# Performance work log

Measured on AMD Instinct MI355X. Metric: run time of the kernel, lower is better.

Reference implementation:

```python
import jax, jax.numpy as jnp
import numpy as np

B, C, T = 128, 272, 1024
D1, K = 270, 32


def setup_inputs() -> dict:
    key = jax.random.key(0)
    k1, k2, k3, k4 = jax.random.split(key, 4)
    X = jax.random.normal(k1, (B, C, T), dtype=jnp.float32)
    loc = jax.random.uniform(k2, (C, 2), dtype=jnp.float32)  # 2D sensor coords in [0,1]
    z_re = jax.random.normal(k3, (D1, K, K), dtype=jnp.float32)
    z_im = jax.random.normal(k4, (D1, K, K), dtype=jnp.float32)
    return {"X": X, "loc": loc, "z_re": z_re, "z_im": z_im}


def reference(X, loc, z_re, z_im):
    # X: [B, C, T]; loc: [C, 2]; z_re/z_im: [D1, K, K]
    Kdim = z_re.shape[1]
    x, y = loc[:, 0], loc[:, 1]                      # [C]
    k = jnp.arange(Kdim, dtype=X.dtype)
    # phase[k, l, c] = 2*pi*(k*x[c] + l*y[c])
    phase = 2.0 * jnp.pi * (k[:, None, None] * x[None, None, :]
                            + k[None, :, None] * y[None, None, :])  # [K, K, C]
    # a[j, c] = sum_{k,l} z_re[j,k,l]*cos(phase) + z_im[j,k,l]*sin(phase)
    A = (jnp.einsum('dkl,klc->dc', z_re, jnp.cos(phase))
         + jnp.einsum('dkl,klc->dc', z_im, jnp.sin(phase)))  # [D1, C]
    # exp(a_j) / sum_c exp(a_j) == softmax over channels (same math)
    w = jax.nn.softmax(A, axis=1)                    # [D1, C]
    # out[b, j, t] = sum_c w[j,c] * X[b,c,t]
    return jnp.einsum('dc,bct->bdt', w, X)           # [B, D1, T]
```

## Files before the change

### kernel.cpp

```cpp
#include <hip/hip_runtime.h>

#define BB 128
#define CC 272
#define TT 1024
#define DD 270
#define KK 32
#define NKC 9
#define MP 272
#define NT 256
#define WCH (CC * KK)
#define WBYTES (NKC * WCH * 2)

typedef __attribute__((ext_vector_type(8))) short s16x8;
typedef __attribute__((ext_vector_type(4))) float f32x4;

__device__ __forceinline__ unsigned short f2bf(float f) {
  unsigned int u = __builtin_bit_cast(unsigned int, f);
  u += 0x7fffu + ((u >> 16) & 1u);
  return (unsigned short)(u >> 16);
}

__global__ __launch_bounds__(288) void phaseA_kernel(
    const float* __restrict__ loc, const float* __restrict__ z_re,
    const float* __restrict__ z_im, float* __restrict__ A) {
  const int d = blockIdx.x;
  const int p = blockIdx.y;
  const int c = threadIdx.x;
  if (c >= CC) return;
  const float TWO_PI = 6.28318530717958647692f;
  float x = loc[2 * c], y = loc[2 * c + 1];
  float sx, cx, sy, cyv;
  sincosf(TWO_PI * x, &sx, &cx);
  sincosf(TWO_PI * y, &sy, &cyv);
  float cl[KK], sl[KK];
  cl[0] = 1.f; sl[0] = 0.f;
#pragma unroll
  for (int l = 1; l < KK; ++l) {
    cl[l] = cl[l - 1] * cyv - sl[l - 1] * sy;
    sl[l] = sl[l - 1] * cyv + cl[l - 1] * sy;
  }
  const int k0 = p * 8;
  float sk, ck;
  sincosf(TWO_PI * (float)k0 * x, &sk, &ck);
  const float* zr = z_re + (size_t)d * (KK * KK) + k0 * KK;
  const float* zi = z_im + (size_t)d * (KK * KK) + k0 * KK;
  float acc = 0.f;
  for (int k = 0; k < 8; ++k) {
    float s_rc = 0.f, s_rs = 0.f, s_ic = 0.f, s_is = 0.f;
#pragma unroll
    for (int l = 0; l < KK; ++l) {
      float vr = zr[k * KK + l];
      float vi = zi[k * KK + l];
      s_rc += vr * cl[l];
      s_rs += vr * sl[l];
      s_ic += vi * cl[l];
      s_is += vi * sl[l];
    }
    acc += ck * (s_rc + s_is) + sk * (s_ic - s_rs);
    float nck = ck * cx - sk * sx;
    sk = sk * cx + ck * sx;
    ck = nck;
  }
  atomicAdd(&A[d * CC + c], acc);
}

__global__ __launch_bounds__(64) void softmax_kernel(
    const float* __restrict__ A, unsigned short* __restrict__ wb) {
  const int d = blockIdx.x;
  const int lane = threadIdx.x;
  const bool live = (d < DD);
  float v[5];
  float inv = 0.f;
  if (live) {
    float m = -3.0e38f;
#pragma unroll
    for (int j = 0; j < 5; ++j) {
      int cidx = lane + 64 * j;
      v[j] = (cidx < CC) ? A[(size_t)d * CC + cidx] : -3.0e38f;
      m = fmaxf(m, v[j]);
    }
#pragma unroll
    for (int off = 32; off >= 1; off >>= 1) m = fmaxf(m, __shfl_xor(m, off, 64));
    float s = 0.f;
#pragma unroll
    for (int j = 0; j < 5; ++j) {
      int cidx = lane + 64 * j;
      v[j] = (cidx < CC) ? expf(v[j] - m) : 0.f;
      s += v[j];
    }
#pragma unroll
    for (int off = 32; off >= 1; off >>= 1) s += __shfl_xor(s, off, 64);
    inv = 1.f / s;
  }
#pragma unroll
  for (int j = 0; j < 5; ++j) {
    int kk = lane + 64 * j;
    if (kk < NKC * KK) {
      unsigned short val = 0;
      if (live && kk < CC) val = f2bf(v[j] * inv);
      int kc = kk >> 5, ks = kk & 31, s = ks >> 3, o = ks & 7;
      wb[(size_t)kc * WCH + d * KK + ((s ^ (d & 3)) << 3) + o] = val;
    }
  }
}

__global__ __launch_bounds__(1024) void gemm_kernel(
    const float* __restrict__ X, const unsigned short* __restrict__ wb,
    float* __restrict__ out) {
  __shared__ unsigned short wlds[NKC * WCH];
  const int bid = blockIdx.x;
  const int b = bid >> 2;
  const int t0 = (bid & 3) * NT;
  const int tid = threadIdx.x;
  const int lane = tid & 63;
  const int wv = tid >> 6;
  const int q = lane >> 4;
  const int r16 = lane & 15;

  {
    const char* src = (const char*)wb;
    char* dst = (char*)wlds;
#pragma unroll
    for (int r = 0; r < 10; ++r) {
      int idx = tid + r * 1024;
      if (idx < WBYTES / 16) {
        __builtin_amdgcn_global_load_lds(
            (const __attribute__((address_space(1))) unsigned int*)(src + idx * 16),
            (__attribute__((address_space(3))) unsigned int*)(dst + idx * 16),
            16, 0, 0);
      }
    }
  }

  f32x4 acc[17];
#pragma unroll
  for (int i = 0; i < 17; ++i) acc[i] = (f32x4){0.f, 0.f, 0.f, 0.f};

  const float* Xb = X + (size_t)b * (CC * TT) + t0 + wv * 16 + r16;
  const int csub = q * 8;
  const int base_l = r16 * 64 + ((q ^ (r16 & 3)) << 4);

  float xf[8];
#pragma unroll
  for (int j = 0; j < 8; ++j) xf[j] = Xb[(size_t)(csub + j) * TT];

  __syncthreads();

  for (int kc = 0; kc < NKC; ++kc) {
    float xn[8];
    if (kc < NKC - 1) {
      const int cbase = (kc + 1) * KK + csub;
#pragma unroll
      for (int j = 0; j < 8; ++j)
        xn[j] = (cbase + j < CC) ? Xb[(size_t)(cbase + j) * TT] : 0.f;
    } else {
#pragma unroll
      for (int j = 0; j < 8; ++j) xn[j] = 0.f;
    }
    union { unsigned int u[4]; s16x8 v; } bf;
#pragma unroll
    for (int j2 = 0; j2 < 4; ++j2)
      bf.u[j2] = (unsigned int)f2bf(xf[2 * j2]) |
                 ((unsigned int)f2bf(xf[2 * j2 + 1]) << 16);
    const char* wchunk = (const char*)wlds + kc * (WCH * 2);
#pragma unroll
    for (int mt = 0; mt < 17; ++mt) {
      s16x8 afrag = *(const s16x8*)(wchunk + mt * 1024 + base_l);
      acc[mt] = __builtin_amdgcn_mfma_f32_16x16x32_bf16(afrag, bf.v, acc[mt], 0, 0, 0);
    }
#pragma unroll
    for (int j = 0; j < 8; ++j) xf[j] = xn[j];
  }

  float* op = out + (size_t)b * (DD * TT) + t0 + wv * 16 + r16;
#pragma unroll
  for (int mt = 0; mt < 17; ++mt) {
#pragma unroll
    for (int r = 0; r < 4; ++r) {
      int drow = mt * 16 + q * 4 + r;
      if (drow < DD) op[(size_t)drow * TT] = acc[mt][r];
    }
  }
}

extern "C" void kernel_launch(void* const* d_in, const int* in_sizes, int n_in,
                              void* d_out, int out_size, void* d_ws, size_t ws_size,
                              hipStream_t stream) {
  const float* X = (const float*)d_in[0];
  const float* loc = (const float*)d_in[1];
  const float* z_re = (const float*)d_in[2];
  const float* z_im = (const float*)d_in[3];
  float* out = (float*)d_out;

  float* A = (float*)d_ws;
  unsigned short* wbf = (unsigned short*)((char*)d_ws + 294912);

  hipMemsetAsync(A, 0, DD * CC * sizeof(float), stream);
  phaseA_kernel<<<dim3(DD, 4), 288, 0, stream>>>(loc, z_re, z_im, A);
  softmax_kernel<<<MP, 64, 0, stream>>>(A, wbf);
  gemm_kernel<<<BB * (TT / NT), 1024, 0, stream>>>(X, wbf, out);
}
```

Baseline: 314.5 us.

## Process two T-tiles per GEMM block and store weights in MFMA fragment order

Each GEMM block now covers 512 time steps as two sequential 256-wide passes, so the bf16 weight matrix is staged into LDS half as often (256 blocks instead of 512). The softmax kernel writes the weights already laid out in MFMA A-fragment order, which turns each LDS read into a contiguous lane*16 access with no XOR swizzle. Between the two passes the accumulators are flushed to global memory. The grid now has 256 blocks, so it barely covers the CU count and leaves less room for overlap across blocks.

Result: slower. 369.4 us (+17.5%).

```diff
diff --git a/kernel.cpp b/kernel.cpp
--- a/kernel.cpp
+++ b/kernel.cpp
@@ -7,8 +7,7 @@
 #define KK 32
 #define NKC 9
 #define MP 272
-#define NT 256
-#define WCH (CC * KK)
+#define WCH (MP * KK)
 #define WBYTES (NKC * WCH * 2)
 
 typedef __attribute__((ext_vector_type(8))) short s16x8;
@@ -92,14 +91,15 @@
     for (int off = 32; off >= 1; off >>= 1) s += __shfl_xor(s, off, 64);
     inv = 1.f / s;
   }
+  const int mt = d >> 4, r = d & 15;
 #pragma unroll
   for (int j = 0; j < 5; ++j) {
     int kk = lane + 64 * j;
     if (kk < NKC * KK) {
       unsigned short val = 0;
       if (live && kk < CC) val = f2bf(v[j] * inv);
-      int kc = kk >> 5, ks = kk & 31, s = ks >> 3, o = ks & 7;
-      wb[(size_t)kc * WCH + d * KK + ((s ^ (d & 3)) << 3) + o] = val;
+      int kc = kk >> 5, q = (kk >> 3) & 3, jj = kk & 7;
+      wb[(size_t)kc * WCH + mt * 512 + q * 128 + r * 8 + jj] = val;
     }
   }
 }
@@ -109,13 +109,14 @@
     float* __restrict__ out) {
   __shared__ unsigned short wlds[NKC * WCH];
   const int bid = blockIdx.x;
-  const int b = bid >> 2;
-  const int t0 = (bid & 3) * NT;
+  const int b = bid >> 1;
+  const int th = (bid & 1) * 512;
   const int tid = threadIdx.x;
   const int lane = tid & 63;
   const int wv = tid >> 6;
   const int q = lane >> 4;
   const int r16 = lane & 15;
+  const int csub = q * 8;
 
   {
     const char* src = (const char*)wb;
@@ -136,23 +137,43 @@
 #pragma unroll
   for (int i = 0; i < 17; ++i) acc[i] = (f32x4){0.f, 0.f, 0.f, 0.f};
 
-  const float* Xb = X + (size_t)b * (CC * TT) + t0 + wv * 16 + r16;
-  const int csub = q * 8;
-  const int base_l = r16 * 64 + ((q ^ (r16 & 3)) << 4);
+  const float* Xb0 = X + (size_t)b * (CC * TT) + th + wv * 16 + r16;
+  float* const ob0 = out + (size_t)b * (DD * TT) + th + wv * 16 + r16;
 
   float xf[8];
 #pragma unroll
-  for (int j = 0; j < 8; ++j) xf[j] = Xb[(size_t)(csub + j) * TT];
+  for (int j = 0; j < 8; ++j) xf[j] = Xb0[(size_t)(csub + j) * TT];
 
   __syncthreads();
 
-  for (int kc = 0; kc < NKC; ++kc) {
+  for (int cl = 0; cl < 18; ++cl) {
+    const int kc = cl - (cl >= 9 ? 9 : 0);
+    if (cl == 9) {
+      float* op = ob0;
+#pragma unroll
+      for (int mt = 0; mt < 17; ++mt) {
+#pragma unroll
+        for (int r = 0; r < 4; ++r) {
+          int drow = mt * 16 + q * 4 + r;
+          if (drow < DD) op[(size_t)drow * TT] = acc[mt][r];
+        }
+      }
+#pragma unroll
+      for (int i = 0; i < 17; ++i) acc[i] = (f32x4){0.f, 0.f, 0.f, 0.f};
+    }
     float xn[8];
-    if (kc < NKC - 1) {
-      const int cbase = (kc + 1) * KK + csub;
-#pragma unroll
-      for (int j = 0; j < 8; ++j)
-        xn[j] = (cbase + j < CC) ? Xb[(size_t)(cbase + j) * TT] : 0.f;
+    if (cl < 17) {
+      const int nl = cl + 1;
+      const int nkc = nl - (nl >= 9 ? 9 : 0);
+      const float* Xb = Xb0 + (nl >= 9 ? 256 : 0);
+      const int cb = nkc * KK + csub;
+      if (nkc == 8 && csub >= 16) {
+#pragma unroll
+        for (int j = 0; j < 8; ++j) xn[j] = 0.f;
+      } else {
+#pragma unroll
+        for (int j = 0; j < 8; ++j) xn[j] = Xb[(size_t)(cb + j) * TT];
+      }
     } else {
 #pragma unroll
       for (int j = 0; j < 8; ++j) xn[j] = 0.f;
@@ -165,14 +186,14 @@
     const char* wchunk = (const char*)wlds + kc * (WCH * 2);
 #pragma unroll
     for (int mt = 0; mt < 17; ++mt) {
-      s16x8 afrag = *(const s16x8*)(wchunk + mt * 1024 + base_l);
+      s16x8 afrag = *(const s16x8*)(wchunk + mt * 1024 + lane * 16);
       acc[mt] = __builtin_amdgcn_mfma_f32_16x16x32_bf16(afrag, bf.v, acc[mt], 0, 0, 0);
     }
 #pragma unroll
     for (int j = 0; j < 8; ++j) xf[j] = xn[j];
   }
 
-  float* op = out + (size_t)b * (DD * TT) + t0 + wv * 16 + r16;
+  float* op = ob0 + 256;
 #pragma unroll
   for (int mt = 0; mt < 17; ++mt) {
 #pragma unroll
@@ -198,5 +219,5 @@
   hipMemsetAsync(A, 0, DD * CC * sizeof(float), stream);
   phaseA_kernel<<<dim3(DD, 4), 288, 0, stream>>>(loc, z_re, z_im, A);
   softmax_kernel<<<MP, 64, 0, stream>>>(A, wbf);
-  gemm_kernel<<<BB * (TT / NT), 1024, 0, stream>>>(X, wbf, out);
-}
+  gemm_kernel<<<BB * 2, 1024, 0, stream>>>(X, wbf, out);
+}
```
